# Optimization experiments

Measured on AMD Instinct MI355X. Metric: run time of the kernel, lower is better.

The kernel has to match this reference:

```python
import jax, jax.numpy as jnp
import numpy as np

T, D_IN, D_OUT, R, S = 8192, 4096, 4096, 16, 16  # tokens, in, out, lora rank, n_stacks
GATE_THRESHOLD = 0.12


def setup_inputs() -> dict:
    key = jax.random.key(0)
    ks = jax.random.split(key, 6)
    x = jax.random.normal(ks[0], (T, D_IN), jnp.float32)
    W = jax.random.normal(ks[1], (D_OUT, D_IN), jnp.float32) * 0.02  # frozen linear weight
    b = jax.random.normal(ks[2], (D_OUT,), jnp.float32) * 0.02       # frozen linear bias
    A = jax.random.normal(ks[3], (S, R, D_IN), jnp.float32) * 0.02   # per-stack lora_A
    B = jax.random.normal(ks[4], (S, D_OUT, R), jnp.float32) * 0.02  # per-stack lora_B
    domain_weights = jax.random.uniform(ks[5], (S,), jnp.float32)    # sigmoid-router weights per domain
    stack_domain = jnp.arange(S, dtype=jnp.int32)                    # stack -> domain index (count=1 each)
    return {"x": x, "W": W, "b": b, "A": A, "B": B,
            "domain_weights": domain_weights, "stack_domain": stack_domain}


def reference(x, W, b, A, B, domain_weights, stack_domain):
    # base frozen linear: out = x @ W^T + b
    base = x @ W.T + b  # [T, D_OUT]
    # threshold-gated per-stack weights: w if w > GATE_THRESHOLD else 0
    g = jnp.where(domain_weights > GATE_THRESHOLD, domain_weights, 0.0)[stack_domain]  # [S]
    # grouped LoRA: stack(x) = (x @ A_s^T) @ B_s^T, combined with gate weights
    h = jnp.einsum('td,srd->str', x, A)          # [S, T, R]
    lora = jnp.einsum('s,str,sor->to', g, h, B)  # [T, D_OUT]
    # original wraps stack contributions in torch.no_grad()
    return base + jax.lax.stop_gradient(lora)
```

## Files before the change

kernel.cpp:

```cpp
#include <hip/hip_runtime.h>
#include <hip/hip_bf16.h>

typedef __bf16 bf16;
typedef __attribute__((ext_vector_type(8))) __bf16 bf16x8;
typedef __attribute__((ext_vector_type(4))) float f32x4;

#define T_TOK 8192
#define DIN   4096
#define DOUT  4096
#define RNK   16
#define NS    16
#define KLORA (NS * RNK)
#define GATE  0.12f

typedef __attribute__((address_space(1))) const void gconst_t;
typedef __attribute__((address_space(3))) void lds_t;

__device__ __forceinline__ void gload_lds16(const void* g, void* l) {
  __builtin_amdgcn_global_load_lds((gconst_t*)g, (lds_t*)l, 16, 0, 0);
}

#define BAR() do { asm volatile("" ::: "memory"); \
                   __builtin_amdgcn_s_barrier();  \
                   asm volatile("" ::: "memory"); } while (0)
#define VMW(n) asm volatile("s_waitcnt vmcnt(" #n ")" ::: "memory")
#define LGKM(n) do { asm volatile("s_waitcnt lgkmcnt(" #n ")" ::: "memory"); \
                     __builtin_amdgcn_sched_barrier(0); } while (0)


__global__ __launch_bounds__(256)
void cast_x_kernel(const float* __restrict__ x, bf16* __restrict__ xb) {
  const long i = ((long)blockIdx.x * 256 + threadIdx.x) * 8;
  const float4 v0 = *(const float4*)(x + i);
  const float4 v1 = *(const float4*)(x + i + 4);
  bf16x8 o;
  o[0] = (bf16)v0.x; o[1] = (bf16)v0.y; o[2] = (bf16)v0.z; o[3] = (bf16)v0.w;
  o[4] = (bf16)v1.x; o[5] = (bf16)v1.y; o[6] = (bf16)v1.z; o[7] = (bf16)v1.w;
  *(bf16x8*)(xb + i) = o;
}

__global__ __launch_bounds__(256)
void build_bg_kernel(const float* __restrict__ B, const float* __restrict__ dw,
                     const int* __restrict__ sd, bf16* __restrict__ bg) {
  const int t = blockIdx.x * 256 + threadIdx.x;
  const int o = t >> 8, k = t & 255, s = k >> 4, r = k & 15;
  const float w = dw[sd[s]];
  const float g = (w > GATE) ? w : 0.f;
  bg[t] = (bf16)(g * B[((size_t)s * DOUT + o) * RNK + r]);
}

__global__ __launch_bounds__(256)
void transpose_a_kernel(const float* __restrict__ A, bf16* __restrict__ at) {
  __shared__ float t[32][33];
  const int d0 = blockIdx.x * 32, k0 = blockIdx.y * 32;
  const int tx = threadIdx.x & 31, ty = threadIdx.x >> 5;
#pragma unroll
  for (int i = 0; i < 32; i += 8)
    t[ty + i][tx] = A[(size_t)(k0 + ty + i) * DIN + d0 + tx];
  __syncthreads();
#pragma unroll
  for (int i = 0; i < 32; i += 8)
    at[(size_t)(d0 + ty + i) * KLORA + k0 + tx] = (bf16)t[tx][ty + i];
}

__global__ __launch_bounds__(256)
void gemm_bt(const bf16* __restrict__ Am, const bf16* __restrict__ Bm,
             const float* __restrict__ extra, bf16* __restrict__ outB,
             int M, int N, int K) {
  constexpr int BM = 128, BN = 128, BK = 32;
  __shared__ __align__(16) bf16 At[BM * BK];
  __shared__ __align__(16) bf16 Bt[BN * BK];

  const int tid  = threadIdx.x;
  const int wave = tid >> 6, lane = tid & 63;

  const int nwg = gridDim.x, bid = blockIdx.x;
  const int qq  = nwg >> 3;
  const int sw  = (bid & 7) * qq + (bid >> 3);
  const int ntN = N / BN;
  const long row0 = (long)(sw / ntN) * BM;
  const long col0 = (long)(sw % ntN) * BN;

  f32x4 acc[4][4] = {};
  const int kSteps = K / BK;

  auto stage = [&](int ks) {
    const long k0 = (long)ks * BK;
#pragma unroll
    for (int r = 0; r < 2; ++r) {
      const int off = tid * 16 + r * 4096;
      const int row = off >> 6;
      const int el  = (off & 63) >> 1;
      char* ldsA = (char*)At + (wave << 10) + (r << 12);
      char* ldsB = (char*)Bt + (wave << 10) + (r << 12);
      gload_lds16(Am + (row0 + row) * K + k0 + el, ldsA);
      gload_lds16(Bm + (col0 + row) * K + k0 + el, ldsB);
    }
  };

  stage(0);
  for (int ks = 0; ks < kSteps; ++ks) {
    __syncthreads();
    bf16x8 afr[4], bfr[4];
    const int koff = (lane >> 4) << 3;
    const int rsel = lane & 15;
    const int wr = wave >> 1, wc = wave & 1;
#pragma unroll
    for (int m = 0; m < 4; ++m)
      afr[m] = *(const bf16x8*)&At[((wr << 6) + (m << 4) + rsel) * BK + koff];
#pragma unroll
    for (int n = 0; n < 4; ++n)
      bfr[n] = *(const bf16x8*)&Bt[((wc << 6) + (n << 4) + rsel) * BK + koff];
    __syncthreads();
    if (ks + 1 < kSteps) stage(ks + 1);
#pragma unroll
    for (int m = 0; m < 4; ++m)
#pragma unroll
      for (int n = 0; n < 4; ++n)
        acc[m][n] = __builtin_amdgcn_mfma_f32_16x16x32_bf16(afr[m], bfr[n],
                                                            acc[m][n], 0, 0, 0);
  }

  const int wr = wave >> 1, wc = wave & 1;
#pragma unroll
  for (int m = 0; m < 4; ++m)
#pragma unroll
    for (int n = 0; n < 4; ++n)
#pragma unroll
      for (int j = 0; j < 4; ++j) {
        const long row = row0 + wr * 64 + m * 16 + ((lane >> 4) << 2) + j;
        const long col = col0 + wc * 64 + n * 16 + (lane & 15);
        outB[row * N + col] = (bf16)(acc[m][n][j] + extra[row * N + col]);
      }
}

__global__ __launch_bounds__(512, 2)
void gemm256(const bf16* __restrict__ Am, const bf16* __restrict__ Bm,
             const float* __restrict__ bias, float* __restrict__ out,
             int M, int N, int K) {
  extern __shared__ char smem[];
  const int tid  = threadIdx.x;
  const int wave = tid >> 6, lane = tid & 63;
  const int wr = wave >> 2, wc = wave & 3;
  const int rsel = lane & 15, klane = lane >> 4;

  const int nwg = gridDim.x, bid = blockIdx.x;
  const int sw  = (bid & 7) * (nwg >> 3) + (bid >> 3);
  const int ntN = N >> 8;
  const long row0 = (long)(sw / ntN) << 8;
  const long col0 = (long)(sw % ntN) << 8;

  long srcA[2], srcB[2];
  int  ldsd[2];
  {
    const int rlo = lane >> 2;
    const int kbe = (((lane & 3) * 16) ^ (((lane >> 5) & 1) << 5)) >> 1;
#pragma unroll
    for (int r = 0; r < 2; ++r) {
      const int row = wave * 32 + r * 16 + rlo;
      srcA[r] = (row0 + row) * (long)K + kbe;
      srcB[r] = (col0 + row) * (long)K + kbe;
      ldsd[r] = (wave * 2 + r) << 10;
    }
  }

  const int nT = K >> 6;

  auto stage_half = [&](int H) {
    if (H >= 4 * nT) return;
    const int  slot = H & 7;
    const long kofs = (long)(H >> 2) * 64 + (long)((H >> 1) & 1) * 32;
    if (H & 1) {
#pragma unroll
      for (int r = 0; r < 2; ++r)
        gload_lds16(Bm + srcB[r] + kofs, smem + (slot << 14) + ldsd[r]);
    } else {
#pragma unroll
      for (int r = 0; r < 2; ++r)
        gload_lds16(Am + srcA[r] + kofs, smem + (slot << 14) + ldsd[r]);
    }
  };

  const int laneoff = rsel * 64 + ((klane * 16) ^ ((rsel & 8) << 2));

  f32x4 acc[8][4] = {};
  bf16x8 afr0[4], afr1[4], bfr0[4], bfr1[4];

  auto readA = [&](int slot, int mh, bf16x8* dst) {
    const char* base = smem + (slot << 14) + ((wr * 128 + mh * 64) << 6) + laneoff;
#pragma unroll
    for (int mi = 0; mi < 4; ++mi)
      dst[mi] = *(const bf16x8*)(base + (mi << 10));
  };
  auto readB = [&](int slot, bf16x8* dst) {
    const char* base = smem + (slot << 14) + ((wc * 64) << 6) + laneoff;
#pragma unroll
    for (int n = 0; n < 4; ++n)
      dst[n] = *(const bf16x8*)(base + (n << 10));
  };
  auto mfma16 = [&](int mh, const bf16x8* a, const bf16x8* bf) {
    __builtin_amdgcn_s_setprio(1);
#pragma unroll
    for (int mi = 0; mi < 4; ++mi)
#pragma unroll
      for (int n = 0; n < 4; ++n)
        acc[mh * 4 + mi][n] = __builtin_amdgcn_mfma_f32_16x16x32_bf16(
            a[mi], bf[n], acc[mh * 4 + mi][n], 0, 0, 0);
    __builtin_amdgcn_s_setprio(0);
  };

  stage_half(0); stage_half(1); stage_half(2); stage_half(3); stage_half(4);
  VMW(6);
  BAR();
  readB(1, bfr0); readA(0, 0, afr0);

  for (int t = 0; t < nT; ++t) {
    const int b  = (t & 1) << 2;
    const int b2 = b ^ 4;
    BAR();
    stage_half(4 * t + 5);
    readA(b | 0, 1, afr1);
    LGKM(4);
    mfma16(0, afr0, bfr0);
    if (t == nT - 1) { VMW(0); } else { VMW(4); }
    BAR();
    stage_half(4 * t + 6);
    readB(b | 3, bfr1); readA(b | 2, 0, afr0);
    LGKM(8);
    mfma16(1, afr1, bfr0);
    BAR();
    stage_half(4 * t + 7);
    readA(b | 2, 1, afr1);
    LGKM(4);
    mfma16(0, afr0, bfr1);
    VMW(4);
    BAR();
    stage_half(4 * t + 8);
    if (t + 1 < nT) {
      readB(b2 | 1, bfr0); readA(b2 | 0, 0, afr0);
      LGKM(8);
    } else {
      LGKM(0);
    }
    mfma16(1, afr1, bfr1);
  }

#pragma unroll
  for (int m = 0; m < 8; ++m)
#pragma unroll
    for (int n = 0; n < 4; ++n)
#pragma unroll
      for (int j = 0; j < 4; ++j) {
        const long row = row0 + wr * 128 + m * 16 + klane * 4 + j;
        const long col = col0 + wc * 64 + n * 16 + rsel;
        out[row * N + col] = acc[m][n][j] + bias[col];
      }
}


extern "C" void kernel_launch(void* const* d_in, const int* in_sizes, int n_in,
                              void* d_out, int out_size, void* d_ws, size_t ws_size,
                              hipStream_t stream) {
  (void)in_sizes; (void)n_in; (void)out_size; (void)ws_size;
  const float* x  = (const float*)d_in[0];
  const float* W  = (const float*)d_in[1];
  const float* b  = (const float*)d_in[2];
  const float* A  = (const float*)d_in[3];
  const float* B  = (const float*)d_in[4];
  const float* dw = (const float*)d_in[5];
  const int*   sd = (const int*)d_in[6];
  float* out = (float*)d_out;

  char* ws = (char*)d_ws;
  bf16* xb    = (bf16*)(ws);
  bf16* weff  = (bf16*)(ws + ((size_t)64 << 20));
  bf16* bg    = (bf16*)(ws + ((size_t)96 << 20));
  bf16* acatT = (bf16*)(ws + ((size_t)98 << 20));

  cast_x_kernel<<<(T_TOK * DIN / 8) / 256, 256, 0, stream>>>(x, xb);
  build_bg_kernel<<<(DOUT * KLORA) / 256, 256, 0, stream>>>(B, dw, sd, bg);
  transpose_a_kernel<<<dim3(DIN / 32, KLORA / 32), 256, 0, stream>>>(A, acatT);

  gemm_bt<<<(DOUT / 128) * (DIN / 128), 256, 0, stream>>>(
      bg, acatT, W, weff, DOUT, DIN, KLORA);

  static_assert((T_TOK % 256) == 0 && (DOUT % 256) == 0 && (DIN % 64) == 0, "");
  hipFuncSetAttribute(reinterpret_cast<const void*>(gemm256),
                      hipFuncAttributeMaxDynamicSharedMemorySize, 131072);
  gemm256<<<(T_TOK / 256) * (DOUT / 256), 512, 131072, stream>>>(
      xb, weff, b, out, T_TOK, DOUT, DIN);
}
```

Baseline: 327.1 us.

## Merge prep kernels into two launches and interleave LDS reads with MFMAs

Folds the B-gating and A-transpose kernels into one launch, and runs the x cast in the same launch as the low-rank W_eff GEMM, cutting four prep launches to two and letting independent work overlap. The main GEMM loop now waits for all LDS reads up front, then issues MFMA groups interleaved one-by-one with the next fragment's LDS reads under sched barriers, to hide LDS latency behind matrix ops. The trade-off is that the full lgkmcnt(0) waits and strict sched barriers may serialize more and limit the compiler's scheduling freedom.

Result: slower. 347.0 us (+6.1%).

```diff
diff --git a/kernel.cpp b/kernel.cpp
--- a/kernel.cpp
+++ b/kernel.cpp
@@ -26,60 +26,47 @@
 #define VMW(n) asm volatile("s_waitcnt vmcnt(" #n ")" ::: "memory")
 #define LGKM(n) do { asm volatile("s_waitcnt lgkmcnt(" #n ")" ::: "memory"); \
                      __builtin_amdgcn_sched_barrier(0); } while (0)
+#define SB0 __builtin_amdgcn_sched_barrier(0)
 
 
 __global__ __launch_bounds__(256)
-void cast_x_kernel(const float* __restrict__ x, bf16* __restrict__ xb) {
-  const long i = ((long)blockIdx.x * 256 + threadIdx.x) * 8;
-  const float4 v0 = *(const float4*)(x + i);
-  const float4 v1 = *(const float4*)(x + i + 4);
-  bf16x8 o;
-  o[0] = (bf16)v0.x; o[1] = (bf16)v0.y; o[2] = (bf16)v0.z; o[3] = (bf16)v0.w;
-  o[4] = (bf16)v1.x; o[5] = (bf16)v1.y; o[6] = (bf16)v1.z; o[7] = (bf16)v1.w;
-  *(bf16x8*)(xb + i) = o;
-}
-
-__global__ __launch_bounds__(256)
-void build_bg_kernel(const float* __restrict__ B, const float* __restrict__ dw,
-                     const int* __restrict__ sd, bf16* __restrict__ bg) {
-  const int t = blockIdx.x * 256 + threadIdx.x;
-  const int o = t >> 8, k = t & 255, s = k >> 4, r = k & 15;
-  const float w = dw[sd[s]];
-  const float g = (w > GATE) ? w : 0.f;
-  bg[t] = (bf16)(g * B[((size_t)s * DOUT + o) * RNK + r]);
-}
-
-__global__ __launch_bounds__(256)
-void transpose_a_kernel(const float* __restrict__ A, bf16* __restrict__ at) {
-  __shared__ float t[32][33];
-  const int d0 = blockIdx.x * 32, k0 = blockIdx.y * 32;
-  const int tx = threadIdx.x & 31, ty = threadIdx.x >> 5;
-#pragma unroll
-  for (int i = 0; i < 32; i += 8)
-    t[ty + i][tx] = A[(size_t)(k0 + ty + i) * DIN + d0 + tx];
-  __syncthreads();
-#pragma unroll
-  for (int i = 0; i < 32; i += 8)
-    at[(size_t)(d0 + ty + i) * KLORA + k0 + tx] = (bf16)t[tx][ty + i];
-}
-
-__global__ __launch_bounds__(256)
-void gemm_bt(const bf16* __restrict__ Am, const bf16* __restrict__ Bm,
-             const float* __restrict__ extra, bf16* __restrict__ outB,
-             int M, int N, int K) {
-  constexpr int BM = 128, BN = 128, BK = 32;
-  __shared__ __align__(16) bf16 At[BM * BK];
-  __shared__ __align__(16) bf16 Bt[BN * BK];
-
+void prep_small_kernel(const float* __restrict__ B, const float* __restrict__ dw,
+                       const int* __restrict__ sd, bf16* __restrict__ bg,
+                       const float* __restrict__ A, bf16* __restrict__ at) {
+  __shared__ float tl[32][33];
+  if (blockIdx.x < 4096) {
+    const int t = blockIdx.x * 256 + threadIdx.x;
+    const int o = t >> 8, k = t & 255, s = k >> 4, r = k & 15;
+    const float w = dw[sd[s]];
+    const float g = (w > GATE) ? w : 0.f;
+    bg[t] = (bf16)(g * B[((size_t)s * DOUT + o) * RNK + r]);
+  } else {
+    const int tb = blockIdx.x - 4096;
+    const int d0 = (tb & 127) * 32, k0 = (tb >> 7) * 32;
+    const int tx = threadIdx.x & 31, ty = threadIdx.x >> 5;
+#pragma unroll
+    for (int i = 0; i < 32; i += 8)
+      tl[ty + i][tx] = A[(size_t)(k0 + ty + i) * DIN + d0 + tx];
+    __syncthreads();
+#pragma unroll
+    for (int i = 0; i < 32; i += 8)
+      at[(size_t)(d0 + ty + i) * KLORA + k0 + tx] = (bf16)tl[tx][ty + i];
+  }
+}
+
+
+__device__ __forceinline__
+void gemm_bt_body(int bid, const bf16* __restrict__ Am, const bf16* __restrict__ Bm,
+                  const float* __restrict__ extra, bf16* __restrict__ outB,
+                  int M, int N, int K, bf16* At, bf16* Bt) {
+  constexpr int BK = 32;
   const int tid  = threadIdx.x;
   const int wave = tid >> 6, lane = tid & 63;
 
-  const int nwg = gridDim.x, bid = blockIdx.x;
-  const int qq  = nwg >> 3;
-  const int sw  = (bid & 7) * qq + (bid >> 3);
-  const int ntN = N / BN;
-  const long row0 = (long)(sw / ntN) * BM;
-  const long col0 = (long)(sw % ntN) * BN;
+  const int sw  = (bid & 7) * 128 + (bid >> 3);
+  const int ntN = N / 128;
+  const long row0 = (long)(sw / ntN) * 128;
+  const long col0 = (long)(sw % ntN) * 128;
 
   f32x4 acc[4][4] = {};
   const int kSteps = K / BK;
@@ -134,6 +121,25 @@
       }
 }
 
+__global__ __launch_bounds__(256)
+void weff_cast_kernel(const bf16* __restrict__ bg, const bf16* __restrict__ acatT,
+                      const float* __restrict__ W, bf16* __restrict__ weff,
+                      const float* __restrict__ x, bf16* __restrict__ xb) {
+  __shared__ __align__(16) bf16 At[128 * 32];
+  __shared__ __align__(16) bf16 Bt[128 * 32];
+  if (blockIdx.x < 1024) {
+    gemm_bt_body(blockIdx.x, bg, acatT, W, weff, DOUT, DIN, KLORA, At, Bt);
+  } else {
+    const long i = ((long)(blockIdx.x - 1024) * 256 + threadIdx.x) * 8;
+    const float4 v0 = *(const float4*)(x + i);
+    const float4 v1 = *(const float4*)(x + i + 4);
+    bf16x8 o;
+    o[0] = (bf16)v0.x; o[1] = (bf16)v0.y; o[2] = (bf16)v0.z; o[3] = (bf16)v0.w;
+    o[4] = (bf16)v1.x; o[5] = (bf16)v1.y; o[6] = (bf16)v1.z; o[7] = (bf16)v1.w;
+    *(bf16x8*)(xb + i) = o;
+  }
+}
+
 __global__ __launch_bounds__(512, 2)
 void gemm256(const bf16* __restrict__ Am, const bf16* __restrict__ Bm,
              const float* __restrict__ bias, float* __restrict__ out,
@@ -186,64 +192,77 @@
   f32x4 acc[8][4] = {};
   bf16x8 afr0[4], afr1[4], bfr0[4], bfr1[4];
 
-  auto readA = [&](int slot, int mh, bf16x8* dst) {
-    const char* base = smem + (slot << 14) + ((wr * 128 + mh * 64) << 6) + laneoff;
-#pragma unroll
-    for (int mi = 0; mi < 4; ++mi)
-      dst[mi] = *(const bf16x8*)(base + (mi << 10));
-  };
-  auto readB = [&](int slot, bf16x8* dst) {
-    const char* base = smem + (slot << 14) + ((wc * 64) << 6) + laneoff;
-#pragma unroll
-    for (int n = 0; n < 4; ++n)
-      dst[n] = *(const bf16x8*)(base + (n << 10));
-  };
-  auto mfma16 = [&](int mh, const bf16x8* a, const bf16x8* bf) {
-    __builtin_amdgcn_s_setprio(1);
-#pragma unroll
-    for (int mi = 0; mi < 4; ++mi)
-#pragma unroll
-      for (int n = 0; n < 4; ++n)
-        acc[mh * 4 + mi][n] = __builtin_amdgcn_mfma_f32_16x16x32_bf16(
-            a[mi], bf[n], acc[mh * 4 + mi][n], 0, 0, 0);
-    __builtin_amdgcn_s_setprio(0);
-  };
+#define RDA(slot, mh, mi, dst) \
+  (dst)[(mi)] = *(const bf16x8*)(smem + ((slot) << 14) + \
+                 (((wr << 7) + (mh) * 64 + (mi) * 16) << 6) + laneoff)
+#define RDB(slot, n, dst) \
+  (dst)[(n)] = *(const bf16x8*)(smem + ((slot) << 14) + \
+                (((wc << 6) + (n) * 16) << 6) + laneoff)
+#define MB(mh, mi, A_, B_) do { \
+  acc[(mh)*4+(mi)][0] = __builtin_amdgcn_mfma_f32_16x16x32_bf16((A_)[(mi)], (B_)[0], acc[(mh)*4+(mi)][0], 0, 0, 0); \
+  acc[(mh)*4+(mi)][1] = __builtin_amdgcn_mfma_f32_16x16x32_bf16((A_)[(mi)], (B_)[1], acc[(mh)*4+(mi)][1], 0, 0, 0); \
+  acc[(mh)*4+(mi)][2] = __builtin_amdgcn_mfma_f32_16x16x32_bf16((A_)[(mi)], (B_)[2], acc[(mh)*4+(mi)][2], 0, 0, 0); \
+  acc[(mh)*4+(mi)][3] = __builtin_amdgcn_mfma_f32_16x16x32_bf16((A_)[(mi)], (B_)[3], acc[(mh)*4+(mi)][3], 0, 0, 0); \
+} while (0)
 
   stage_half(0); stage_half(1); stage_half(2); stage_half(3); stage_half(4);
   VMW(6);
   BAR();
-  readB(1, bfr0); readA(0, 0, afr0);
+  RDB(1, 0, bfr0); RDB(1, 1, bfr0); RDB(1, 2, bfr0); RDB(1, 3, bfr0);
+  RDA(0, 0, 0, afr0); RDA(0, 0, 1, afr0); RDA(0, 0, 2, afr0); RDA(0, 0, 3, afr0);
 
   for (int t = 0; t < nT; ++t) {
     const int b  = (t & 1) << 2;
     const int b2 = b ^ 4;
+    const bool last = (t == nT - 1);
     BAR();
     stage_half(4 * t + 5);
-    readA(b | 0, 1, afr1);
-    LGKM(4);
-    mfma16(0, afr0, bfr0);
-    if (t == nT - 1) { VMW(0); } else { VMW(4); }
+    LGKM(0);
+    __builtin_amdgcn_s_setprio(1);
+    MB(0, 0, afr0, bfr0); SB0; RDA(b | 0, 1, 0, afr1); SB0;
+    MB(0, 1, afr0, bfr0); SB0; RDA(b | 0, 1, 1, afr1); SB0;
+    MB(0, 2, afr0, bfr0); SB0; RDA(b | 0, 1, 2, afr1); SB0;
+    MB(0, 3, afr0, bfr0); SB0; RDA(b | 0, 1, 3, afr1);
+    __builtin_amdgcn_s_setprio(0);
+    if (last) { VMW(0); } else { VMW(4); }
     BAR();
     stage_half(4 * t + 6);
-    readB(b | 3, bfr1); readA(b | 2, 0, afr0);
-    LGKM(8);
-    mfma16(1, afr1, bfr0);
+    LGKM(0);
+    __builtin_amdgcn_s_setprio(1);
+    MB(1, 0, afr1, bfr0); SB0; RDB(b | 3, 0, bfr1); RDB(b | 3, 1, bfr1); SB0;
+    MB(1, 1, afr1, bfr0); SB0; RDB(b | 3, 2, bfr1); RDB(b | 3, 3, bfr1); SB0;
+    MB(1, 2, afr1, bfr0); SB0; RDA(b | 2, 0, 0, afr0); RDA(b | 2, 0, 1, afr0); SB0;
+    MB(1, 3, afr1, bfr0); SB0; RDA(b | 2, 0, 2, afr0); RDA(b | 2, 0, 3, afr0);
+    __builtin_amdgcn_s_setprio(0);
     BAR();
     stage_half(4 * t + 7);
-    readA(b | 2, 1, afr1);
-    LGKM(4);
-    mfma16(0, afr0, bfr1);
+    LGKM(0);
+    __builtin_amdgcn_s_setprio(1);
+    MB(0, 0, afr0, bfr1); SB0; RDA(b | 2, 1, 0, afr1); SB0;
+    MB(0, 1, afr0, bfr1); SB0; RDA(b | 2, 1, 1, afr1); SB0;
+    MB(0, 2, afr0, bfr1); SB0; RDA(b | 2, 1, 2, afr1); SB0;
+    MB(0, 3, afr0, bfr1); SB0; RDA(b | 2, 1, 3, afr1);
+    __builtin_amdgcn_s_setprio(0);
     VMW(4);
     BAR();
     stage_half(4 * t + 8);
-    if (t + 1 < nT) {
-      readB(b2 | 1, bfr0); readA(b2 | 0, 0, afr0);
-      LGKM(8);
+    LGKM(0);
+    __builtin_amdgcn_s_setprio(1);
+    if (!last) {
+      MB(1, 0, afr1, bfr1); SB0; RDB(b2 | 1, 0, bfr0); RDB(b2 | 1, 1, bfr0); SB0;
+      MB(1, 1, afr1, bfr1); SB0; RDB(b2 | 1, 2, bfr0); RDB(b2 | 1, 3, bfr0); SB0;
+      MB(1, 2, afr1, bfr1); SB0; RDA(b2 | 0, 0, 0, afr0); RDA(b2 | 0, 0, 1, afr0); SB0;
+      MB(1, 3, afr1, bfr1); SB0; RDA(b2 | 0, 0, 2, afr0); RDA(b2 | 0, 0, 3, afr0);
     } else {
-      LGKM(0);
+      MB(1, 0, afr1, bfr1); MB(1, 1, afr1, bfr1);
+      MB(1, 2, afr1, bfr1); MB(1, 3, afr1, bfr1);
     }
-    mfma16(1, afr1, bfr1);
-  }
+    __builtin_amdgcn_s_setprio(0);
+  }
+
+#undef RDA
+#undef RDB
+#undef MB
 
 #pragma unroll
   for (int m = 0; m < 8; ++m)
@@ -277,12 +296,10 @@
   bf16* bg    = (bf16*)(ws + ((size_t)96 << 20));
   bf16* acatT = (bf16*)(ws + ((size_t)98 << 20));
 
-  cast_x_kernel<<<(T_TOK * DIN / 8) / 256, 256, 0, stream>>>(x, xb);
-  build_bg_kernel<<<(DOUT * KLORA) / 256, 256, 0, stream>>>(B, dw, sd, bg);
-  transpose_a_kernel<<<dim3(DIN / 32, KLORA / 32), 256, 0, stream>>>(A, acatT);
-
-  gemm_bt<<<(DOUT / 128) * (DIN / 128), 256, 0, stream>>>(
-      bg, acatT, W, weff, DOUT, DIN, KLORA);
+  prep_small_kernel<<<4096 + 1024, 256, 0, stream>>>(B, dw, sd, bg, A, acatT);
+
+  weff_cast_kernel<<<1024 + (T_TOK * DIN / 8) / 256, 256, 0, stream>>>(
+      bg, acatT, W, weff, x, xb);
 
   static_assert((T_TOK % 256) == 0 && (DOUT % 256) == 0 && (DIN % 64) == 0, "");
   hipFuncSetAttribute(reinterpret_cast<const void*>(gemm256),
```
